# Performance work log

Hardware: AMD Instinct MI355X
Metric: run time of the kernel (lower is better)

## Reference

```python
import jax, jax.numpy as jnp
import numpy as np

ALPHA = 4.0  # spikingjelly default Sigmoid surrogate alpha
BN_EPS = 1e-5

@jax.custom_vjp
def spike(x):
    return (x >= 0.0).astype(x.dtype)

def _spike_fwd(x):
    return spike(x), x

def _spike_bwd(res, g):
    s = jax.nn.sigmoid(ALPHA * res)
    return (g * ALPHA * s * (1.0 - s),)

spike.defvjp(_spike_fwd, _spike_bwd)

def lif(x, tau=2.0, vth=1.0):
    # MultiStepLIFNode: hard reset (v_reset=0), detach_reset=True, scan over time axis 0
    def step(v, xt):
        h = v + (xt - v) / tau          # charge
        s = spike(h - vth)              # fire (surrogate grad)
        v_next = h * (1.0 - jax.lax.stop_gradient(s))  # detached hard reset to 0
        return v_next, s
    _, out = jax.lax.scan(step, jnp.zeros_like(x[0]), x)
    return out

def conv_bn(x, w, b, g, be, m, var):
    # x: [TB, C, N]; 1x1 Conv1d is a channel GEMM, then eval-mode BatchNorm1d
    y = jnp.einsum('oc,bcn->bon', w, x) + b[None, :, None]
    inv = g / jnp.sqrt(var + BN_EPS)
    return (y - m[None, :, None]) * inv[None, :, None] + be[None, :, None]

def setup_inputs() -> dict:
    key = jax.random.key(0)
    T, B, C, H, W = 4, 32, 512, 14, 14
    ks = jax.random.split(key, 32)
    d = {'x': jax.random.normal(ks[0], (T, B, C, H, W), dtype=jnp.float32)}
    scale = 1.0 / np.sqrt(C)
    i = 1
    for p in ['q', 'k', 'v', 'p']:
        d[p + '_cw'] = jax.random.normal(ks[i], (C, C), dtype=jnp.float32) * scale; i += 1
        d[p + '_cb'] = jax.random.normal(ks[i], (C,), dtype=jnp.float32) * 0.1; i += 1
        d[p + '_bg'] = jnp.ones((C,), dtype=jnp.float32)
        d[p + '_bb'] = jnp.zeros((C,), dtype=jnp.float32)
        d[p + '_bm'] = jax.random.normal(ks[i], (C,), dtype=jnp.float32) * 0.1; i += 1
        d[p + '_bv'] = jax.random.uniform(ks[i], (C,), dtype=jnp.float32, minval=0.5, maxval=1.5); i += 1
    d['push_w'] = jnp.asarray(1.0, dtype=jnp.float32)
    d['pull_w'] = jnp.asarray(1.0, dtype=jnp.float32)
    d['pp_bias'] = jnp.asarray(0.0, dtype=jnp.float32)
    return d

def reference(x,
              q_cw, q_cb, q_bg, q_bb, q_bm, q_bv,
              k_cw, k_cb, k_bg, k_bb, k_bm, k_bv,
              v_cw, v_cb, v_bg, v_bb, v_bm, v_bv,
              p_cw, p_cb, p_bg, p_bb, p_bm, p_bv,
              push_w, pull_w, pp_bias):
    T, B, C, H, W = x.shape
    N = H * W
    nh = 8
    hd = C // nh
    scale = 0.125

    xs = lif(x)                                   # head_lif, [T,B,C,H,W]
    xf = xs.reshape(T * B, C, N)
    q = conv_bn(xf, q_cw, q_cb, q_bg, q_bb, q_bm, q_bv).reshape(T, B, C, N)
    k = conv_bn(xf, k_cw, k_cb, k_bg, k_bb, k_bm, k_bv).reshape(T, B, C, N)
    v = conv_bn(xf, v_cw, v_cb, v_bg, v_bb, v_bm, v_bv).reshape(T, B, C, N)

    q_on = lif(q)
    q_off = lif(-q)

    def to_heads(t):  # [T,B,C,N] -> [T,B,nh,N,hd]
        return jnp.swapaxes(t, -1, -2).reshape(T, B, N, nh, hd).transpose(0, 1, 3, 2, 4)

    q_on_h = to_heads(q_on)
    q_off_h = to_heads(q_off)
    k_h = to_heads(lif(k))
    v_h = to_heads(lif(v))

    pw = jax.nn.softplus(push_w)
    pl = jax.nn.softplus(pull_w)
    diff = pw * q_on_h - pl * q_off_h + pp_bias   # push-pull gating
    q_pp = lif(diff)

    kv = jnp.einsum('tbhnd,tbhne->tbhde', k_h, v_h)      # k^T @ v, [T,B,h,hd,hd]
    o = jnp.einsum('tbhnd,tbhde->tbhne', q_pp, kv) * scale

    o = o.transpose(0, 1, 2, 4, 3).reshape(T, B, C, N)   # transpose(3,4) then merge heads
    o = lif(o, vth=0.5)                                   # attn_lif
    o = conv_bn(o.reshape(T * B, C, N), p_cw, p_cb, p_bg, p_bb, p_bm, p_bv)
    return o.reshape(T, B, C, H, W)
```

## Files before the change

### kernel.cpp

```cpp
#include <hip/hip_runtime.h>
#include <hip/hip_bf16.h>
#include <math.h>

typedef unsigned short u16;
typedef unsigned int   u32;

#define CC 512
#define NN 196
#define TT 4
#define BB 32
#define TBB 128
#define NHH 8
#define HD 64

#define ROWS_T  6272
#define CSTRIDE ((size_t)ROWS_T * CC)

typedef __attribute__((ext_vector_type(8))) _Float16 f16x8;
typedef __attribute__((ext_vector_type(4))) float f32x4;

#define ONE_H 0x3C00

__device__ __forceinline__ u16 h_bits(_Float16 h) { return *(u16*)&h; }
__device__ __forceinline__ float h2f(u16 u) { return (float)(*(const _Float16*)&u); }
__device__ __forceinline__ u32 pk2(u16 a, u16 b) { return (u32)a | ((u32)b << 16); }

__device__ __forceinline__ void gld16(const void* g, void* l) {
    __builtin_amdgcn_global_load_lds(
        (const __attribute__((address_space(1))) void*)g,
        (__attribute__((address_space(3))) void*)l, 16, 0, 0);
}

__global__ __launch_bounds__(256) void k_prep(
    const float* __restrict__ qw, const float* __restrict__ kw,
    const float* __restrict__ vw, const float* __restrict__ pw,
    const float* __restrict__ cb0, const float* __restrict__ bg0, const float* __restrict__ bb0,
    const float* __restrict__ bm0, const float* __restrict__ bv0,
    const float* __restrict__ cb1, const float* __restrict__ bg1, const float* __restrict__ bb1,
    const float* __restrict__ bm1, const float* __restrict__ bv1,
    const float* __restrict__ cb2, const float* __restrict__ bg2, const float* __restrict__ bb2,
    const float* __restrict__ bm2, const float* __restrict__ bv2,
    const float* __restrict__ cb3, const float* __restrict__ bg3, const float* __restrict__ bb3,
    const float* __restrict__ bm3, const float* __restrict__ bv3,
    u16* __restrict__ W2, float* __restrict__ SS, float* __restrict__ SH) {
    if (blockIdx.x < 4096) {
        size_t idx = (size_t)blockIdx.x * 256 + threadIdx.x;
        int g = (int)(idx >> 18);
        size_t rem = idx & 262143;
        const float* Ws = (g == 0) ? qw : (g == 1) ? kw : (g == 2) ? vw : pw;
        float w  = Ws[rem];
        _Float16 h0 = (fabsf(w) < 6.2e-5f) ? (_Float16)0.0f : (_Float16)w;
        float r = (w - (float)h0) * 2048.0f;
        _Float16 h1 = (_Float16)r;
        size_t base = (size_t)g * 524288 + rem;
        W2[base] = h_bits(h0); W2[base + 262144] = h_bits(h1);
        return;
    }
    int idx = (blockIdx.x - 4096) * 256 + threadIdx.x;
    int g = idx >> 9, o = idx & 511;
    const float* cb = g == 0 ? cb0 : g == 1 ? cb1 : g == 2 ? cb2 : cb3;
    const float* bg = g == 0 ? bg0 : g == 1 ? bg1 : g == 2 ? bg2 : bg3;
    const float* bb = g == 0 ? bb0 : g == 1 ? bb1 : g == 2 ? bb2 : bb3;
    const float* bm = g == 0 ? bm0 : g == 1 ? bm1 : g == 2 ? bm2 : bm3;
    const float* bv = g == 0 ? bv0 : g == 1 ? bv1 : g == 2 ? bv2 : bv3;
    float inv = bg[o] / sqrtf(bv[o] + 1e-5f);
    SS[g * 512 + o] = inv;
    SH[g * 512 + o] = (cb[o] - bm[o]) * inv + bb[o];
}

__global__ __launch_bounds__(256) void k_head_lif(const float* __restrict__ x, u16* __restrict__ XS) {
    __shared__ float T[64][65];
    const int tid = threadIdx.x;
    const int n0 = blockIdx.x * 64;
    const int b  = blockIdx.y;
    const int c_base = blockIdx.z * 64;
    const int c_l = tid >> 4;
    const int n4  = (tid & 15) * 4;
    const bool lv = (n0 + n4) < NN;
    const int n_r = tid >> 2;
    const int cq  = (tid & 3) * 16;
    const bool wv = (n0 + n_r) < NN;

    float v[4][4];
    #pragma unroll
    for (int k = 0; k < 4; ++k)
        #pragma unroll
        for (int j = 0; j < 4; ++j) v[k][j] = 0.f;

    for (int t = 0; t < TT; ++t) {
        const size_t xb = ((size_t)(t * BB + b) * CC + c_base) * NN;
        float s[4][4];
        #pragma unroll
        for (int k = 0; k < 4; ++k) {
            const int c = c_l + 16 * k;
            float4 xv = make_float4(0.f, 0.f, 0.f, 0.f);
            if (lv) xv = *(const float4*)(x + xb + (size_t)c * NN + n0 + n4);
            float xa[4] = {xv.x, xv.y, xv.z, xv.w};
            #pragma unroll
            for (int j = 0; j < 4; ++j) {
                float h = v[k][j] + (xa[j] - v[k][j]) * 0.5f;
                s[k][j] = (h >= 1.f) ? 1.f : 0.f;
                v[k][j] = (h >= 1.f) ? 0.f : h;
            }
        }
        __syncthreads();
        #pragma unroll
        for (int k = 0; k < 4; ++k)
            #pragma unroll
            for (int j = 0; j < 4; ++j) T[c_l + 16 * k][n4 + j] = s[k][j];
        __syncthreads();
        if (wv) {
            const size_t ob = ((size_t)(t * BB + b) * NN + n0 + n_r) * CC + c_base + cq;
            u16 u[16];
            #pragma unroll
            for (int m = 0; m < 16; ++m) u[m] = (T[cq + m][n_r] != 0.f) ? ONE_H : 0;
            uint4 q0 = make_uint4(pk2(u[0],u[1]),  pk2(u[2],u[3]),  pk2(u[4],u[5]),  pk2(u[6],u[7]));
            uint4 q1 = make_uint4(pk2(u[8],u[9]),  pk2(u[10],u[11]),pk2(u[12],u[13]),pk2(u[14],u[15]));
            *(uint4*)(XS + ob)     = q0;
            *(uint4*)(XS + ob + 8) = q1;
        }
        __syncthreads();
    }
}

__global__ __launch_bounds__(256) void k_gemm_qkv(const u16* __restrict__ S, const u16* __restrict__ W2,
                                                  const float* __restrict__ scale, const float* __restrict__ shift,
                                                  u16* __restrict__ QS, u16* __restrict__ KS, u16* __restrict__ VS,
                                                  const float* __restrict__ PW, const float* __restrict__ PL,
                                                  const float* __restrict__ PB) {
    __shared__ __align__(16) u16 smem[24576];
    u16* Xt  = smem;
    u16* WtF = smem + 8192;
    const int tid  = threadIdx.x;
    const int lane = tid & 63;
    const int w    = tid >> 6;
    const int bid  = blockIdx.x;
    const int work = (bid & 7) * 294 + (bid >> 3);
    const int rrt  = work / 12;
    const int gw   = work - rrt * 12;
    const int g    = gw >> 2;
    const int wtile = gw & 3;
    const int rr0  = rrt * 32;
    const u16* Wb = W2 + (size_t)g * 524288 + (size_t)(wtile * 128) * CC;
    const float* scl = scale + g * 512;
    const float* shf = shift + g * 512;

    const int lrow8  = lane >> 3;
    const int gchunk = ((lane & 7) ^ lrow8) * 8;
    const int l15 = lane & 15;
    const int q4  = lane >> 4;
    const int wm = (w >> 1) * 64, wn = (w & 1) * 64;

    const size_t arow0 = (size_t)w * CSTRIDE + (size_t)rr0 * CC;

    f32x4 acc[4][4];
    f32x4 zz = {0.f, 0.f, 0.f, 0.f};
    #pragma unroll
    for (int i = 0; i < 4; ++i)
        #pragma unroll
        for (int j = 0; j < 4; ++j) acc[i][j] = zz;

    for (int c0 = 0; c0 < CC; c0 += 64) {
        __syncthreads();
        #pragma unroll
        for (int i = 0; i < 4; ++i) {
            int p = w * 4 + i;
            gld16(S + arow0 + (size_t)(i * 8 + lrow8) * CC + c0 + gchunk, &Xt[p * 512]);
        }
        #pragma unroll
        for (int i = 0; i < 8; ++i) {
            int lin = w * 8 + i;
            int s = lin >> 4, p = lin & 15;
            gld16(Wb + (size_t)s * 262144 + (size_t)(p * 8 + lrow8) * CC + c0 + gchunk,
                  WtF + s * 8192 + p * 512);
        }
        __syncthreads();

        #pragma unroll
        for (int ks = 0; ks < 2; ++ks) {
            const int cpo = ((ks * 4 + q4) ^ (l15 & 7)) * 8;
            f16x8 sf[4], sflo[4];
            #pragma unroll
            for (int i = 0; i < 4; ++i) {
                sf[i]   = *(const f16x8*)&Xt[(wm + i * 16 + l15) * 64 + cpo];
                sflo[i] = sf[i] * (_Float16)0.00048828125f;
            }
            #pragma unroll
            for (int s = 0; s < 2; ++s) {
                f16x8 wf[4];
                #pragma unroll
                for (int i = 0; i < 4; ++i)
                    wf[i] = *(const f16x8*)&WtF[s * 8192 + (wn + i * 16 + l15) * 64 + cpo];
                #pragma unroll
                for (int mt = 0; mt < 4; ++mt)
                    #pragma unroll
                    for (int nt = 0; nt < 4; ++nt)
                        acc[mt][nt] = __builtin_amdgcn_mfma_f32_16x16x32_f16(
                            s ? sflo[mt] : sf[mt], wf[nt], acc[mt][nt], 0, 0, 0);
            }
        }
    }

    const float pwv = (g == 0) ? log1pf(expf(PW[0])) : 0.f;
    const float plv = (g == 0) ? log1pf(expf(PL[0])) : 0.f;
    const float pbv = (g == 0) ? PB[0] : 0.f;
    u16* OUT = (g == 0) ? QS : (g == 1) ? KS : VS;
    float* LY = (float*)smem;
    const int pairid = w & 1;
    const int pr  = tid >> 7;
    const int idx = tid & 127;

    #pragma unroll
    for (int cc = 0; cc < 2; ++cc) {
        __syncthreads();
        #pragma unroll
        for (int ntl = 0; ntl < 2; ++ntl) {
            const int nt = cc * 2 + ntl;
            const int o  = wtile * 128 + wn + nt * 16 + l15;
            const float sc = scl[o], sh = shf[o];
            const int col32 = ntl * 16 + l15;
            #pragma unroll
            for (int mt = 0; mt < 4; ++mt) {
                const int tr0 = wm + mt * 16 + q4 * 4;
                #pragma unroll
                for (int r = 0; r < 4; ++r)
                    LY[(pairid * 128 + tr0 + r) * 33 + col32] = acc[mt][nt][r] * sc + sh;
            }
        }
        __syncthreads();
        #pragma unroll
        for (int stp = 0; stp < 4; ++stp) {
            const int chain = stp * 128 + idx;
            const int nn  = chain >> 4;
            const int c2  = (chain & 15) * 2;
            const int rr  = rr0 + nn;
            const float* Lp = &LY[(pr * 128 + nn) * 33 + c2];
            float ya[4][2];
            #pragma unroll
            for (int t = 0; t < 4; ++t) {
                ya[t][0] = Lp[t * 32 * 33];
                ya[t][1] = Lp[t * 32 * 33 + 1];
            }
            const int ocol = wtile * 128 + pr * 64 + cc * 32 + c2;
            u32* op = (u32*)(OUT + (size_t)rr * CC + ocol);
            if (g == 0) {
                float von[2] = {0.f, 0.f}, voff[2] = {0.f, 0.f}, vpp[2] = {0.f, 0.f};
                #pragma unroll
                for (int t = 0; t < 4; ++t) {
                    u16 sp2[2];
                    #pragma unroll
                    for (int j = 0; j < 2; ++j) {
                        float qv = ya[t][j], h;
                        h = von[j]  + ( qv - von[j] ) * 0.5f; bool s1 = (h >= 1.f); von[j]  = s1 ? 0.f : h;
                        h = voff[j] + (-qv - voff[j]) * 0.5f; bool s2 = (h >= 1.f); voff[j] = s2 ? 0.f : h;
                        float diff = pwv * (s1 ? 1.f : 0.f) - plv * (s2 ? 1.f : 0.f) + pbv;
                        h = vpp[j] + (diff - vpp[j]) * 0.5f; bool sp = (h >= 1.f); vpp[j] = sp ? 0.f : h;
                        sp2[j] = sp ? ONE_H : 0;
                    }
                    op[t * (CSTRIDE / 2)] = pk2(sp2[0], sp2[1]);
                }
            } else {
                float vm[2] = {0.f, 0.f};
                #pragma unroll
                for (int t = 0; t < 4; ++t) {
                    u16 s2[2];
                    #pragma unroll
                    for (int j = 0; j < 2; ++j) {
                        float h = vm[j] + (ya[t][j] - vm[j]) * 0.5f;
                        bool s = (h >= 1.f); vm[j] = s ? 0.f : h;
                        s2[j] = s ? ONE_H : 0;
                    }
                    op[t * (CSTRIDE / 2)] = pk2(s2[0], s2[1]);
                }
            }
        }
    }
}

__global__ __launch_bounds__(256) void k_attn(const u16* __restrict__ Q, const u16* __restrict__ K,
                                              const u16* __restrict__ V, u16* __restrict__ OS) {
    __shared__ __align__(16) u16 sm[19584];
    u16* Kt  = sm;
    u16* Vt  = sm + 8704;
    u16* Qs  = sm;
    u16* kvT = sm + 14976;

    const int tid = threadIdx.x;
    const int tb  = blockIdx.x >> 3;
    const int h   = blockIdx.x & 7;
    const size_t gb = (size_t)tb * NN * CC + (size_t)h * HD;

    const int srow = tid >> 2;
    const int sdq  = (tid & 3) * 16;

    const int lane = tid & 63;
    const int w    = tid >> 6;
    const int l15  = lane & 15;
    const int kb8  = (lane >> 4) * 8;
    const int quad = (lane >> 4) * 4;
    const int dh = (w >> 1) * 32, eh = (w & 1) * 32;

    f32x4 accA[2][2];
    f32x4 zz = {0.f, 0.f, 0.f, 0.f};
    #pragma unroll
    for (int i = 0; i < 2; ++i)
        #pragma unroll
        for (int j = 0; j < 2; ++j) accA[i][j] = zz;

    const uint4 z4 = make_uint4(0, 0, 0, 0);

    #pragma unroll
    for (int ch = 0; ch < 2; ++ch) {
        if (ch) __syncthreads();
        #pragma unroll
        for (int c = 0; c < 2; ++c) {
            int n  = ch * 128 + c * 64 + srow;
            int nl = c * 64 + srow;
            bool valid = n < NN;
            const u16* kr = K + gb + (size_t)n * CC + sdq;
            const u16* vr = V + gb + (size_t)n * CC + sdq;
            uint4 ka  = valid ? *(const uint4*)kr : z4;
            uint4 kb2 = valid ? *(const uint4*)(kr + 8) : z4;
            uint4 va  = valid ? *(const uint4*)vr : z4;
            uint4 vb2 = valid ? *(const uint4*)(vr + 8) : z4;
            u32 kwv[8] = {ka.x, ka.y, ka.z, ka.w, kb2.x, kb2.y, kb2.z, kb2.w};
            u32 vwv[8] = {va.x, va.y, va.z, va.w, vb2.x, vb2.y, vb2.z, vb2.w};
            #pragma unroll
            for (int i = 0; i < 8; ++i) {
                Kt[(sdq + 2 * i) * 136 + nl]     = (u16)(kwv[i] & 0xFFFF);
                Kt[(sdq + 2 * i + 1) * 136 + nl] = (u16)(kwv[i] >> 16);
                Vt[(sdq + 2 * i) * 136 + nl]     = (u16)(vwv[i] & 0xFFFF);
                Vt[(sdq + 2 * i + 1) * 136 + nl] = (u16)(vwv[i] >> 16);
            }
        }
        __syncthreads();
        #pragma unroll
        for (int k0 = 0; k0 < 128; k0 += 32) {
            f16x8 af[2], bv[2];
            #pragma unroll
            for (int i = 0; i < 2; ++i) {
                af[i] = *(const f16x8*)&Kt[(dh + i * 16 + l15) * 136 + k0 + kb8];
                bv[i] = *(const f16x8*)&Vt[(eh + i * 16 + l15) * 136 + k0 + kb8];
            }
            #pragma unroll
            for (int i = 0; i < 2; ++i)
                #pragma unroll
                for (int j = 0; j < 2; ++j)
                    accA[i][j] = __builtin_amdgcn_mfma_f32_16x16x32_f16(af[i], bv[j], accA[i][j], 0, 0, 0);
        }
    }
    __syncthreads();

    #pragma unroll
    for (int i = 0; i < 2; ++i)
        #pragma unroll
        for (int j = 0; j < 2; ++j)
            #pragma unroll
            for (int r = 0; r < 4; ++r) {
                int e = eh + j * 16 + l15;
                int d = dh + i * 16 + quad + r;
                _Float16 hv = (_Float16)accA[i][j][r];
                kvT[e * 72 + d] = h_bits(hv);
            }
    #pragma unroll
    for (int p = 0; p < 4; ++p) {
        int n = p * 64 + srow;
        if (n < 208) {
            if (n < NN) {
                const u16* qr = Q + gb + (size_t)n * CC + sdq;
                uint4 qa  = *(const uint4*)qr;
                uint4 qb2 = *(const uint4*)(qr + 8);
                u32 qwv[8] = {qa.x, qa.y, qa.z, qa.w, qb2.x, qb2.y, qb2.z, qb2.w};
                #pragma unroll
                for (int i = 0; i < 8; ++i) {
                    Qs[n * 72 + sdq + 2 * i]     = (u16)(qwv[i] & 0xFFFF);
                    Qs[n * 72 + sdq + 2 * i + 1] = (u16)(qwv[i] >> 16);
                }
            } else {
                #pragma unroll
                for (int i = 0; i < 16; ++i) Qs[n * 72 + sdq + i] = 0;
            }
        }
    }
    __syncthreads();

    f16x8 bq0 = *(const f16x8*)&kvT[(w * 16 + l15) * 72 + 0  + kb8];
    f16x8 bq1 = *(const f16x8*)&kvT[(w * 16 + l15) * 72 + 32 + kb8];
    u16* ob = OS + (size_t)tb * NN * CC + (size_t)h * HD + w * 16 + l15;
    #pragma unroll
    for (int nt = 0; nt < 13; ++nt) {
        f32x4 acc = zz;
        f16x8 a0 = *(const f16x8*)&Qs[(nt * 16 + l15) * 72 + 0  + kb8];
        f16x8 a1 = *(const f16x8*)&Qs[(nt * 16 + l15) * 72 + 32 + kb8];
        acc = __builtin_amdgcn_mfma_f32_16x16x32_f16(a0, bq0, acc, 0, 0, 0);
        acc = __builtin_amdgcn_mfma_f32_16x16x32_f16(a1, bq1, acc, 0, 0, 0);
        #pragma unroll
        for (int r = 0; r < 4; ++r) {
            int n = nt * 16 + quad + r;
            if (n < NN) {
                _Float16 ov = (_Float16)(acc[r] * 0.125f);
                ob[(size_t)n * CC] = h_bits(ov);
            }
        }
    }
}

__global__ __launch_bounds__(256) void k_attn_lif(uint4* __restrict__ OS) {
    const size_t idx = (size_t)blockIdx.x * 256 + threadIdx.x;
    float v[8];
    #pragma unroll
    for (int j = 0; j < 8; ++j) v[j] = 0.f;
    #pragma unroll
    for (int t = 0; t < TT; ++t) {
        const size_t o8 = idx + (size_t)t * (CSTRIDE / 8);
        uint4 d = OS[o8];
        u32 dw[4] = {d.x, d.y, d.z, d.w};
        u16 u[8];
        #pragma unroll
        for (int p = 0; p < 4; ++p) {
            #pragma unroll
            for (int hf = 0; hf < 2; ++hf) {
                int j = p * 2 + hf;
                u16 raw = hf ? (u16)(dw[p] >> 16) : (u16)(dw[p] & 0xFFFF);
                float xv = h2f(raw);
                float h = v[j] + (xv - v[j]) * 0.5f;
                bool s = (h >= 0.5f);
                v[j] = s ? 0.f : h;
                u[j] = s ? ONE_H : 0;
            }
        }
        OS[o8] = make_uint4(pk2(u[0],u[1]), pk2(u[2],u[3]), pk2(u[4],u[5]), pk2(u[6],u[7]));
    }
}

__global__ __launch_bounds__(256) void k_gemm_proj(const u16* __restrict__ S, const u16* __restrict__ W2,
                                                   const float* __restrict__ scale, const float* __restrict__ shift,
                                                   float* __restrict__ Y) {
    __shared__ __align__(16) u16 Xt[128 * 64];
    __shared__ __align__(16) u16 Wt[2][128 * 64];
    const int tid  = threadIdx.x;
    const int lane = tid & 63;
    const int w    = tid >> 6;
    const int bid  = blockIdx.x;
    const int work = (bid & 7) * 98 + (bid >> 3);
    const int ntile = work >> 2;
    const int wtile = work & 3;
    const u16* Sb = S + (size_t)ntile * 128 * CC;
    const u16* Wb = W2 + (size_t)(wtile * 128) * CC;

    const int lrow8  = lane >> 3;
    const int gchunk = ((lane & 7) ^ lrow8) * 8;
    const int l15 = lane & 15;
    const int q4  = lane >> 4;
    const int wm = (w >> 1) * 64, wn = (w & 1) * 64;

    const int tb0 = (ntile * 128) / NN;
    const int bnd = (tb0 + 1) * NN;

    f32x4 acc[4][4];
    f32x4 zz = {0.f, 0.f, 0.f, 0.f};
    #pragma unroll
    for (int i = 0; i < 4; ++i)
        #pragma unroll
        for (int j = 0; j < 4; ++j) acc[i][j] = zz;

    for (int c0 = 0; c0 < CC; c0 += 64) {
        __syncthreads();
        #pragma unroll
        for (int i = 0; i < 4; ++i) {
            int p = w * 4 + i;
            gld16(Sb + (size_t)(p * 8 + lrow8) * CC + c0 + gchunk, &Xt[p * 512]);
        }
        #pragma unroll
        for (int i = 0; i < 8; ++i) {
            int lin = w * 8 + i;
            int s = lin >> 4, p = lin & 15;
            gld16(Wb + (size_t)s * 262144 + (size_t)(p * 8 + lrow8) * CC + c0 + gchunk,
                  &Wt[s][p * 512]);
        }
        __syncthreads();

        #pragma unroll
        for (int ks = 0; ks < 2; ++ks) {
            const int cpo = ((ks * 4 + q4) ^ (l15 & 7)) * 8;
            f16x8 sf[4], sflo[4];
            #pragma unroll
            for (int i = 0; i < 4; ++i) {
                sf[i]   = *(const f16x8*)&Xt[(wn + i * 16 + l15) * 64 + cpo];
                sflo[i] = sf[i] * (_Float16)0.00048828125f;
            }
            #pragma unroll
            for (int s = 0; s < 2; ++s) {
                f16x8 wf[4];
                #pragma unroll
                for (int i = 0; i < 4; ++i)
                    wf[i] = *(const f16x8*)&Wt[s][(wm + i * 16 + l15) * 64 + cpo];
                #pragma unroll
                for (int mt = 0; mt < 4; ++mt)
                    #pragma unroll
                    for (int nt = 0; nt < 4; ++nt)
                        acc[mt][nt] = __builtin_amdgcn_mfma_f32_16x16x32_f16(
                            wf[mt], s ? sflo[nt] : sf[nt], acc[mt][nt], 0, 0, 0);
            }
        }
    }

    #pragma unroll
    for (int mt = 0; mt < 4; ++mt) {
        int o0 = wtile * 128 + wm + mt * 16 + (lane >> 4) * 4;
        #pragma unroll
        for (int nt = 0; nt < 4; ++nt) {
            int row = ntile * 128 + wn + nt * 16 + l15;
            int tb = (row >= bnd) ? tb0 + 1 : tb0;
            int n  = row - tb * NN;
            #pragma unroll
            for (int r = 0; r < 4; ++r)
                Y[((size_t)tb * CC + o0 + r) * NN + n] = acc[mt][nt][r] * scale[o0 + r] + shift[o0 + r];
        }
    }
}

extern "C" void kernel_launch(void* const* d_in, const int* in_sizes, int n_in,
                              void* d_out, int out_size, void* d_ws, size_t ws_size,
                              hipStream_t stream) {
    const float* x    = (const float*)d_in[0];
    const float* q_cw = (const float*)d_in[1];
    const float* q_cb = (const float*)d_in[2];
    const float* q_bg = (const float*)d_in[3];
    const float* q_bb = (const float*)d_in[4];
    const float* q_bm = (const float*)d_in[5];
    const float* q_bv = (const float*)d_in[6];
    const float* k_cw = (const float*)d_in[7];
    const float* k_cb = (const float*)d_in[8];
    const float* k_bg = (const float*)d_in[9];
    const float* k_bb = (const float*)d_in[10];
    const float* k_bm = (const float*)d_in[11];
    const float* k_bv = (const float*)d_in[12];
    const float* v_cw = (const float*)d_in[13];
    const float* v_cb = (const float*)d_in[14];
    const float* v_bg = (const float*)d_in[15];
    const float* v_bb = (const float*)d_in[16];
    const float* v_bm = (const float*)d_in[17];
    const float* v_bv = (const float*)d_in[18];
    const float* p_cw = (const float*)d_in[19];
    const float* p_cb = (const float*)d_in[20];
    const float* p_bg = (const float*)d_in[21];
    const float* p_bb = (const float*)d_in[22];
    const float* p_bm = (const float*)d_in[23];
    const float* p_bv = (const float*)d_in[24];
    const float* pshw = (const float*)d_in[25];
    const float* pllw = (const float*)d_in[26];
    const float* ppb  = (const float*)d_in[27];
    float* out = (float*)d_out;

    if (ws_size < (size_t)242 * 1024 * 1024) return;
    char* W = (char*)d_ws;
    u16*   XS = (u16*)W;
    u16*   QS = (u16*)(W + ((size_t)27 << 20));
    u16*   OS = (u16*)(W + ((size_t)78 << 20));
    u16*   KS = (u16*)(W + ((size_t)182 << 20));
    u16*   VS = (u16*)(W + ((size_t)208 << 20));
    u16*   W2 = (u16*)(W + ((size_t)234 << 20));
    float* SS = (float*)(W + ((size_t)238 << 20));
    float* SH = SS + 2048;

    k_prep<<<4104, 256, 0, stream>>>(q_cw, k_cw, v_cw, p_cw,
                                     q_cb, q_bg, q_bb, q_bm, q_bv,
                                     k_cb, k_bg, k_bb, k_bm, k_bv,
                                     v_cb, v_bg, v_bb, v_bm, v_bv,
                                     p_cb, p_bg, p_bb, p_bm, p_bv, W2, SS, SH);

    k_head_lif<<<dim3(4, 32, 8), 256, 0, stream>>>(x, XS);

    k_gemm_qkv<<<2352, 256, 0, stream>>>(XS, W2, SS, SH, QS, KS, VS, pshw, pllw, ppb);

    k_attn<<<TBB * NHH, 256, 0, stream>>>(QS, KS, VS, OS);
    k_attn_lif<<<1568, 256, 0, stream>>>((uint4*)OS);

    k_gemm_proj<<<784, 256, 0, stream>>>(OS, W2 + 3 * 524288, SS + 1536, SH + 1536, out);
}
```

Baseline: 321.6 us.

## Fuse attention-output LIF into projection GEMM tile loads

Removes the standalone attn_lif kernel and applies the LIF time scan in shared memory inside the projection GEMM. Each row tile now gathers 32 spatial rows across all 4 timesteps, so the scan over T runs on the loaded tile. This cuts a full read and write pass over the attention output and one launch. In exchange it adds an extra barrier and scan work per K-chunk, and the output row mapping changes. Each element's LIF is recomputed by the 4 weight tiles that share the rows.

```diff
diff --git a/kernel.cpp b/kernel.cpp
--- a/kernel.cpp
+++ b/kernel.cpp
@@ -405,34 +405,6 @@
     }
 }
 
-__global__ __launch_bounds__(256) void k_attn_lif(uint4* __restrict__ OS) {
-    const size_t idx = (size_t)blockIdx.x * 256 + threadIdx.x;
-    float v[8];
-    #pragma unroll
-    for (int j = 0; j < 8; ++j) v[j] = 0.f;
-    #pragma unroll
-    for (int t = 0; t < TT; ++t) {
-        const size_t o8 = idx + (size_t)t * (CSTRIDE / 8);
-        uint4 d = OS[o8];
-        u32 dw[4] = {d.x, d.y, d.z, d.w};
-        u16 u[8];
-        #pragma unroll
-        for (int p = 0; p < 4; ++p) {
-            #pragma unroll
-            for (int hf = 0; hf < 2; ++hf) {
-                int j = p * 2 + hf;
-                u16 raw = hf ? (u16)(dw[p] >> 16) : (u16)(dw[p] & 0xFFFF);
-                float xv = h2f(raw);
-                float h = v[j] + (xv - v[j]) * 0.5f;
-                bool s = (h >= 0.5f);
-                v[j] = s ? 0.f : h;
-                u[j] = s ? ONE_H : 0;
-            }
-        }
-        OS[o8] = make_uint4(pk2(u[0],u[1]), pk2(u[2],u[3]), pk2(u[4],u[5]), pk2(u[6],u[7]));
-    }
-}
-
 __global__ __launch_bounds__(256) void k_gemm_proj(const u16* __restrict__ S, const u16* __restrict__ W2,
                                                    const float* __restrict__ scale, const float* __restrict__ shift,
                                                    float* __restrict__ Y) {
@@ -443,9 +415,9 @@
     const int w    = tid >> 6;
     const int bid  = blockIdx.x;
     const int work = (bid & 7) * 98 + (bid >> 3);
-    const int ntile = work >> 2;
+    const int rrt  = work >> 2;
     const int wtile = work & 3;
-    const u16* Sb = S + (size_t)ntile * 128 * CC;
+    const int rr0  = rrt * 32;
     const u16* Wb = W2 + (size_t)(wtile * 128) * CC;
 
     const int lrow8  = lane >> 3;
@@ -454,8 +426,11 @@
     const int q4  = lane >> 4;
     const int wm = (w >> 1) * 64, wn = (w & 1) * 64;
 
-    const int tb0 = (ntile * 128) / NN;
-    const int bnd = (tb0 + 1) * NN;
+    const size_t arow0 = (size_t)w * CSTRIDE + (size_t)rr0 * CC;
+
+    const int nnc = tid >> 3;
+    const int jc  = tid & 7;
+    const int px  = nnc & 7;
 
     f32x4 acc[4][4];
     f32x4 zz = {0.f, 0.f, 0.f, 0.f};
@@ -464,12 +439,14 @@
         #pragma unroll
         for (int j = 0; j < 4; ++j) acc[i][j] = zz;
 
+    u32* X32 = (u32*)Xt;
+
     for (int c0 = 0; c0 < CC; c0 += 64) {
         __syncthreads();
         #pragma unroll
         for (int i = 0; i < 4; ++i) {
             int p = w * 4 + i;
-            gld16(Sb + (size_t)(p * 8 + lrow8) * CC + c0 + gchunk, &Xt[p * 512]);
+            gld16(S + arow0 + (size_t)(i * 8 + lrow8) * CC + c0 + gchunk, &Xt[p * 512]);
         }
         #pragma unroll
         for (int i = 0; i < 8; ++i) {
@@ -481,6 +458,24 @@
         __syncthreads();
 
         #pragma unroll
+        for (int k = 0; k < 4; ++k) {
+            const int pc   = (((jc >> 2) + 2 * k) ^ px);
+            const int cofs = pc * 4 + (jc & 3);
+            float va = 0.f, vb = 0.f;
+            #pragma unroll
+            for (int t = 0; t < 4; ++t) {
+                const int ai = (t * 32 + nnc) * 32 + cofs;
+                u32 d = X32[ai];
+                float xa = h2f((u16)(d & 0xFFFF));
+                float xb = h2f((u16)(d >> 16));
+                float ha = va + (xa - va) * 0.5f; bool sa = (ha >= 0.5f); va = sa ? 0.f : ha;
+                float hb = vb + (xb - vb) * 0.5f; bool sb = (hb >= 0.5f); vb = sb ? 0.f : hb;
+                X32[ai] = pk2(sa ? ONE_H : 0, sb ? ONE_H : 0);
+            }
+        }
+        __syncthreads();
+
+        #pragma unroll
         for (int ks = 0; ks < 2; ++ks) {
             const int cpo = ((ks * 4 + q4) ^ (l15 & 7)) * 8;
             f16x8 sf[4], sflo[4];
@@ -507,12 +502,15 @@
 
     #pragma unroll
     for (int mt = 0; mt < 4; ++mt) {
-        int o0 = wtile * 128 + wm + mt * 16 + (lane >> 4) * 4;
+        int o0 = wtile * 128 + wm + mt * 16 + q4 * 4;
         #pragma unroll
         for (int nt = 0; nt < 4; ++nt) {
-            int row = ntile * 128 + wn + nt * 16 + l15;
-            int tb = (row >= bnd) ? tb0 + 1 : tb0;
-            int n  = row - tb * NN;
+            int row = wn + nt * 16 + l15;
+            int t   = row >> 5;
+            int rr  = rr0 + (row & 31);
+            int b   = rr / NN;
+            int n   = rr - b * NN;
+            int tb  = t * BB + b;
             #pragma unroll
             for (int r = 0; r < 4; ++r)
                 Y[((size_t)tb * CC + o0 + r) * NN + n] = acc[mt][nt][r] * scale[o0 + r] + shift[o0 + r];
@@ -575,7 +573,6 @@
     k_gemm_qkv<<<2352, 256, 0, stream>>>(XS, W2, SS, SH, QS, KS, VS, pshw, pllw, ppb);
 
     k_attn<<<TBB * NHH, 256, 0, stream>>>(QS, KS, VS, OS);
-    k_attn_lif<<<1568, 256, 0, stream>>>((uint4*)OS);
 
     k_gemm_proj<<<784, 256, 0, stream>>>(OS, W2 + 3 * 524288, SS + 1536, SH + 1536, out);
 }
```

Result: no change. 326.5 us (+1.5%).
